# Kernel tuning notes

Hardware: AMD Instinct MI355X
Metric: run time of the kernel (lower is better)

## Reference

```python
import jax, jax.numpy as jnp
import numpy as np

NUM_NODES = 64   # EEG channels / input size
D = 512          # rnn1 hidden size
N_LAYERS = 3
B, T = 32, 1024


def _lstm_dir(x, W_ih, W_hh, b_ih, b_hh, reverse=False):
    """Single-direction LSTM layer (torch gate order i,f,g,o).
    x: [B,T,I], W_ih: [4H,I], W_hh: [4H,H], biases: [4H]. Returns [B,T,H]."""
    H = W_hh.shape[1]
    # Precompute input projection for all timesteps (big GEMM, compute-bound).
    xp = jnp.einsum('bti,gi->btg', x, W_ih) + (b_ih + b_hh)  # [B,T,4H]

    def step(carry, xt):
        h, c = carry
        gates = xt + h @ W_hh.T                 # [B,4H]
        i, f, g, o = jnp.split(gates, 4, axis=-1)
        i = jax.nn.sigmoid(i)
        f = jax.nn.sigmoid(f)
        g = jnp.tanh(g)
        o = jax.nn.sigmoid(o)
        c = f * c + i * g
        h = o * jnp.tanh(c)
        return (h, c), h

    init = (jnp.zeros((x.shape[0], H), x.dtype), jnp.zeros((x.shape[0], H), x.dtype))
    _, hs = jax.lax.scan(step, init, jnp.swapaxes(xp, 0, 1), reverse=reverse)
    return jnp.swapaxes(hs, 0, 1)  # [B,T,H]


def _bilstm(x, W_ih, W_hh, b_ih, b_hh):
    """Bidirectional layer; params stacked on leading dir axis [2,...]."""
    fwd = _lstm_dir(x, W_ih[0], W_hh[0], b_ih[0], b_hh[0], reverse=False)
    bwd = _lstm_dir(x, W_ih[1], W_hh[1], b_ih[1], b_hh[1], reverse=True)
    return jnp.concatenate([fwd, bwd], axis=-1)  # [B,T,2H]


def setup_inputs() -> dict:
    key = jax.random.key(0)
    ks = jax.random.split(key, 16)
    k1 = 1.0 / np.sqrt(D)          # torch LSTM init bound for rnn1
    k2 = 1.0 / np.sqrt(NUM_NODES)  # for rnn2
    u = lambda k, shape, b: jax.random.uniform(k, shape, jnp.float32, -b, b)
    inp = {
        'x': jax.random.normal(ks[0], (B, T, NUM_NODES), jnp.float32),
        # rnn1 layer 0: input NUM_NODES, 2 directions
        'W_ih_l0': u(ks[1], (2, 4 * D, NUM_NODES), k1),
        'W_hh_l0': u(ks[2], (2, 4 * D, D), k1),
        'b_ih_l0': u(ks[3], (2, 4 * D), k1),
        'b_hh_l0': u(ks[4], (2, 4 * D), k1),
        # rnn1 layers 1-2: input 2*D, stacked [layer, dir, ...]
        'W_ih_l12': u(ks[5], (2, 2, 4 * D, 2 * D), k1),
        'W_hh_l12': u(ks[6], (2, 2, 4 * D, D), k1),
        'b_ih_l12': u(ks[7], (2, 2, 4 * D), k1),
        'b_hh_l12': u(ks[8], (2, 2, 4 * D), k1),
        # rnn2: single unidirectional layer, input 2*D, hidden NUM_NODES
        'W_ih2': u(ks[9], (4 * NUM_NODES, 2 * D), k2),
        'W_hh2': u(ks[10], (4 * NUM_NODES, NUM_NODES), k2),
        'b_ih2': u(ks[11], (4 * NUM_NODES,), k2),
        'b_hh2': u(ks[12], (4 * NUM_NODES,), k2),
    }
    return inp


def reference(x, W_ih_l0, W_hh_l0, b_ih_l0, b_hh_l0,
              W_ih_l12, W_hh_l12, b_ih_l12, b_hh_l12,
              W_ih2, W_hh2, b_ih2, b_hh2):
    out = _bilstm(x, W_ih_l0, W_hh_l0, b_ih_l0, b_hh_l0)        # [B,T,2D]
    for l in range(N_LAYERS - 1):
        out = _bilstm(out, W_ih_l12[l], W_hh_l12[l], b_ih_l12[l], b_hh_l12[l])
    out = _lstm_dir(out, W_ih2, W_hh2, b_ih2, b_hh2)            # [B,T,NUM_NODES]
    return out * 40.0
```

## Files before the change

kernel.cpp:

```cpp
#include <hip/hip_runtime.h>
#include <stdio.h>
#include <stdint.h>

#define BB 32
#define TT 1024
#define DH 512
#define ND 64
#define TC 128

typedef short bf16x8 __attribute__((ext_vector_type(8)));
typedef float f32x4  __attribute__((ext_vector_type(4)));

static __device__ __forceinline__ float bf2f(unsigned short u) {
    union { unsigned int i; float f; } v; v.i = ((unsigned int)u) << 16; return v.f;
}
static __device__ __forceinline__ unsigned short f2bf_rne(float f) {
    union { float f; unsigned int i; } v; v.f = f;
    unsigned int u = v.i;
    return (unsigned short)((u + 0x7fffu + ((u >> 16) & 1u)) >> 16);
}
static __device__ __forceinline__ float sigm(float x) { return 1.f / (1.f + __expf(-x)); }
static __device__ __forceinline__ float tanhs(float x) {
    float ax = fabsf(x);
    float e = __expf(-2.f * ax);
    float t = (1.f - e) / (1.f + e);
    return x < 0.f ? -t : t;
}

__global__ void k_f2bf(const float* __restrict__ src, unsigned short* __restrict__ dst, int n4) {
    int i = blockIdx.x * blockDim.x + threadIdx.x;
    if (i < n4) {
        float4 v = ((const float4*)src)[i];
        ushort4 o;
        o.x = f2bf_rne(v.x); o.y = f2bf_rne(v.y); o.z = f2bf_rne(v.z); o.w = f2bf_rne(v.w);
        ((ushort4*)dst)[i] = o;
    }
}

__global__ void k_bsum(const float* __restrict__ a, const float* __restrict__ b,
                       float* __restrict__ d, int n) {
    int i = blockIdx.x * blockDim.x + threadIdx.x;
    if (i < n) d[i] = a[i] + b[i];
}

__global__ __launch_bounds__(256) void k_gemm(
    const unsigned short* __restrict__ A,
    const unsigned short* __restrict__ W,
    const float* __restrict__ bias,
    unsigned short* __restrict__ out,
    int N, int K)
{
    __shared__ unsigned short lw[128 * 72];
    __shared__ unsigned short la[128 * 72];
    const int tid = threadIdx.x;
    const int n0 = blockIdx.x * 128;
    const int m0 = blockIdx.y * 128;
    const int lane = tid & 63, wv = tid >> 6;
    const int q = lane >> 4, lr = lane & 15;
    const int wn = wv & 1, wm = wv >> 1;

    f32x4 acc[4][4];
#pragma unroll
    for (int i = 0; i < 4; i++)
#pragma unroll
        for (int j = 0; j < 4; j++) acc[i][j] = (f32x4){0.f, 0.f, 0.f, 0.f};

    const int srow = tid >> 1, shalf = tid & 1;
    for (int k0 = 0; k0 < K; k0 += 64) {
        const uint4* gw = (const uint4*)(W + (size_t)(n0 + srow) * K + k0 + shalf * 32);
        const uint4* ga = (const uint4*)(A + (size_t)(m0 + srow) * K + k0 + shalf * 32);
        uint4 wld[4], ald[4];
#pragma unroll
        for (int j = 0; j < 4; j++) { wld[j] = gw[j]; ald[j] = ga[j]; }
        __syncthreads();
#pragma unroll
        for (int j = 0; j < 4; j++) {
            ((uint4*)lw)[srow * 9 + shalf * 4 + j] = wld[j];
            ((uint4*)la)[srow * 9 + shalf * 4 + j] = ald[j];
        }
        __syncthreads();
#pragma unroll
        for (int ks = 0; ks < 2; ks++) {
            bf16x8 fw[4], fa[4];
#pragma unroll
            for (int i = 0; i < 4; i++)
                fw[i] = *(const bf16x8*)&lw[(64 * wn + 16 * i + lr) * 72 + ks * 32 + q * 8];
#pragma unroll
            for (int j = 0; j < 4; j++)
                fa[j] = *(const bf16x8*)&la[(64 * wm + 16 * j + lr) * 72 + ks * 32 + q * 8];
#pragma unroll
            for (int i = 0; i < 4; i++)
#pragma unroll
                for (int j = 0; j < 4; j++)
                    acc[i][j] = __builtin_amdgcn_mfma_f32_16x16x32_bf16(fw[i], fa[j], acc[i][j], 0, 0, 0);
        }
    }
#pragma unroll
    for (int i = 0; i < 4; i++) {
        const int nb = n0 + 64 * wn + 16 * i + q * 4;
        const float4 bb = *(const float4*)(bias + nb);
#pragma unroll
        for (int j = 0; j < 4; j++) {
            const int m = m0 + 64 * wm + 16 * j + lr;
            const int rowp = ((m & 1023) << 5) | (m >> 10);
            ushort4 o;
            o.x = f2bf_rne(acc[i][j][0] + bb.x);
            o.y = f2bf_rne(acc[i][j][1] + bb.y);
            o.z = f2bf_rne(acc[i][j][2] + bb.z);
            o.w = f2bf_rne(acc[i][j][3] + bb.w);
            *(ushort4*)(out + (size_t)rowp * N + nb) = o;
        }
    }
}

__global__ __launch_bounds__(512) void k_layer(
    const unsigned short* A,
    const unsigned short* wih,
    const float* bias,
    const unsigned short* whh,
    unsigned short* __restrict__ outb,
    unsigned short* xpc,
    unsigned short* hbuf,
    unsigned int* ctl, int K)
{
    extern __shared__ unsigned short smem[];
    const int tid = threadIdx.x;
    const int bid = blockIdx.x;
    unsigned int* chunkready = ctl;
    unsigned int* rnnprog = ctl + 128;
    unsigned int* stepflag = ctl + 256;

    if (bid < 64) {
        unsigned short* lw = smem;
        unsigned short* lh = smem + 128 * 520;
        float* lg = (float*)(smem + 128 * 520 + 16 * 520);
        const int dir = bid & 1;
        const int bg = (bid >> 1) & 1;
        const int cs = bid >> 2;
        const int c0 = cs * 32, b0 = bg * 16;
        const int lane = tid & 63, wv = tid >> 6;
        const int q = lane >> 4, lr = lane & 15;

        for (int i = tid; i < 128 * 64; i += 512) {
            int row = i >> 6, ch = i & 63;
            int ty = row >> 5, cc = row & 31;
            ((uint4*)lw)[row * 65 + ch] =
                *(const uint4*)(whh + ((size_t)(dir * 2048 + ty * 512 + c0 + cc) * 512 + ch * 8));
        }
        const int xb = tid >> 5;
        const int xc = tid & 31;
        float cstate = 0.f;
        unsigned int* myflag = stepflag + ((dir * 2 + bg) * 16 + cs) * 16;
        const unsigned int* grpflag = stepflag + (dir * 2 + bg) * 256;
        __syncthreads();

        for (int s = 0; s < TT; ++s) {
            if ((s & (TC - 1)) == 0) {
                const int c = s >> 7;
                if (tid == 0) {
                    while (__hip_atomic_load(&chunkready[c * 16], __ATOMIC_RELAXED,
                                             __HIP_MEMORY_SCOPE_AGENT) < 128u)
                        __builtin_amdgcn_s_sleep(8);
                }
                __syncthreads();
                __builtin_amdgcn_fence(__ATOMIC_ACQUIRE, "agent");
            }
            const unsigned short* xpb = xpc + (size_t)((s >> 7) & 1) * (TC * 32ull * 4096);
            const int t = dir ? (TT - 1 - s) : s;
            const unsigned short* xpp = xpb + ((size_t)((s & (TC - 1)) * 32 + b0 + xb) * 4096)
                                       + dir * 2048 + c0 + xc;
            unsigned short x0 = xpp[0], x1 = xpp[512], x2 = xpp[1024], x3 = xpp[1536];

            if (s > 0) {
                if (wv == 0) {
                    const unsigned int tgt = (unsigned int)s;
                    const unsigned int* fl = grpflag + (lane & 15) * 16;
                    for (;;) {
                        unsigned int v = (lane < 16)
                            ? __hip_atomic_load(fl, __ATOMIC_RELAXED, __HIP_MEMORY_SCOPE_AGENT)
                            : tgt;
                        if (__all((int)(v >= tgt))) break;
                    }
                }
                __syncthreads();
                {
                    const int pp = (s & 1) ^ 1;
                    const unsigned short* hb = hbuf + ((size_t)(dir * 2 + pp) * 32 + b0) * 512;
                    const int ch = tid & 127, r0 = tid >> 7;
                    unsigned long long hv4[4];
#pragma unroll
                    for (int k2 = 0; k2 < 4; ++k2)
                        hv4[k2] = __hip_atomic_load(
                            (const unsigned long long*)(hb + (r0 + k2 * 4) * 512 + ch * 4),
                            __ATOMIC_RELAXED, __HIP_MEMORY_SCOPE_AGENT);
#pragma unroll
                    for (int k2 = 0; k2 < 4; ++k2)
                        *(unsigned long long*)&((unsigned int*)lh)[(r0 + k2 * 4) * 260 + ch * 2] = hv4[k2];
                }
                __syncthreads();
                f32x4 acc = (f32x4){0.f, 0.f, 0.f, 0.f};
                const unsigned short* lwr = lw + (16 * wv + lr) * 520;
                const unsigned short* lhr = lh + lr * 520;
#pragma unroll
                for (int ks = 0; ks < 16; ++ks) {
                    bf16x8 a = *(const bf16x8*)(lwr + ks * 32 + q * 8);
                    bf16x8 b = *(const bf16x8*)(lhr + ks * 32 + q * 8);
                    acc = __builtin_amdgcn_mfma_f32_16x16x32_bf16(a, b, acc, 0, 0, 0);
                }
#pragma unroll
                for (int r = 0; r < 4; ++r)
                    lg[(16 * wv + q * 4 + r) * 17 + lr] = acc[r];
                __syncthreads();
            }

            unsigned short h16;
            {
                float gi = bf2f(x0) + (s > 0 ? lg[(0 * 32 + xc) * 17 + xb] : 0.f);
                float gf = bf2f(x1) + (s > 0 ? lg[(1 * 32 + xc) * 17 + xb] : 0.f);
                float gg = bf2f(x2) + (s > 0 ? lg[(2 * 32 + xc) * 17 + xb] : 0.f);
                float go = bf2f(x3) + (s > 0 ? lg[(3 * 32 + xc) * 17 + xb] : 0.f);
                float ig = sigm(gi), fg = sigm(gf), cg = tanhs(gg), og = sigm(go);
                cstate = fg * cstate + ig * cg;
                float h = og * tanhs(cstate);
                h16 = f2bf_rne(h);
                unsigned int hv = h16;
                unsigned int other = __shfl_xor((int)hv, 1);
                if ((tid & 1) == 0) {
                    size_t idx = ((size_t)(dir * 2 + (s & 1)) * 32 + b0 + xb) * 512 + c0 + xc;
                    unsigned int packed = hv | (other << 16);
                    __hip_atomic_store((unsigned int*)hbuf + (idx >> 1), packed,
                                       __ATOMIC_RELAXED, __HIP_MEMORY_SCOPE_AGENT);
                }
            }
            __syncthreads();
            if (tid == 0)
                __hip_atomic_store(myflag, (unsigned int)(s + 1),
                                   __ATOMIC_RELAXED, __HIP_MEMORY_SCOPE_AGENT);
            if ((s & (TC - 1)) == (TC - 1) && tid == 0)
                __hip_atomic_fetch_add(rnnprog, 1u, __ATOMIC_RELAXED, __HIP_MEMORY_SCOPE_AGENT);
            outb[((size_t)(b0 + xb) * TT + t) * 1024 + dir * 512 + c0 + xc] = h16;
        }
    } else {
        const int w = bid - 64;
        const int engine = tid >> 8;
        const int etid = tid & 255;
        unsigned short* lw = smem + engine * 18432;
        unsigned short* la = lw + 9216;
        const int lane = etid & 63, wv = etid >> 6;
        const int q = lane >> 4, lr = lane & 15;
        const int wn = wv & 1, wm = wv >> 1;
        const int srow = etid >> 1, shalf = etid & 1;

        for (int c = 0; c < 8; ++c) {
            if (c >= 2) {
                if (tid == 0) {
                    unsigned int tgt = 64u * (unsigned int)(c - 1);
                    while (__hip_atomic_load(rnnprog, __ATOMIC_RELAXED,
                                             __HIP_MEMORY_SCOPE_AGENT) < tgt)
                        __builtin_amdgcn_s_sleep(8);
                }
                __syncthreads();
            }
            unsigned short* xpb = xpc + (size_t)(c & 1) * (TC * 32ull * 4096);
            for (int jt = 0; jt < 4; ++jt) {
                const int tau = (w * 2 + engine) + 256 * jt;
                const int dir = tau >> 9, rem = tau & 511;
                const int b = rem >> 4, nx = rem & 15;
                const int t0 = dir ? (TT - c * TC - TC) : (c * TC);
                const int n0 = dir * 2048 + nx * 128;
                const int m0 = b * TT + t0;
                f32x4 acc[4][4];
#pragma unroll
                for (int i = 0; i < 4; i++)
#pragma unroll
                    for (int j = 0; j < 4; j++) acc[i][j] = (f32x4){0.f, 0.f, 0.f, 0.f};

                for (int k0 = 0; k0 < K; k0 += 64) {
                    const uint4* gw = (const uint4*)(wih + (size_t)(n0 + srow) * K + k0 + shalf * 32);
                    const uint4* ga = (const uint4*)(A + (size_t)(m0 + srow) * K + k0 + shalf * 32);
                    uint4 wld[4], ald[4];
#pragma unroll
                    for (int j = 0; j < 4; j++) { wld[j] = gw[j]; ald[j] = ga[j]; }
                    __syncthreads();
#pragma unroll
                    for (int j = 0; j < 4; j++) {
                        ((uint4*)lw)[srow * 9 + shalf * 4 + j] = wld[j];
                        ((uint4*)la)[srow * 9 + shalf * 4 + j] = ald[j];
                    }
                    __syncthreads();
#pragma unroll
                    for (int ks = 0; ks < 2; ks++) {
                        bf16x8 fw[4], fa[4];
#pragma unroll
                        for (int i = 0; i < 4; i++)
                            fw[i] = *(const bf16x8*)&lw[(64 * wn + 16 * i + lr) * 72 + ks * 32 + q * 8];
#pragma unroll
                        for (int j = 0; j < 4; j++)
                            fa[j] = *(const bf16x8*)&la[(64 * wm + 16 * j + lr) * 72 + ks * 32 + q * 8];
#pragma unroll
                        for (int i = 0; i < 4; i++)
#pragma unroll
                            for (int j = 0; j < 4; j++)
                                acc[i][j] = __builtin_amdgcn_mfma_f32_16x16x32_bf16(fw[i], fa[j], acc[i][j], 0, 0, 0);
                    }
                }
#pragma unroll
                for (int i = 0; i < 4; i++) {
                    const int nb = n0 + 64 * wn + 16 * i + q * 4;
                    const float4 bb = *(const float4*)(bias + nb);
#pragma unroll
                    for (int j = 0; j < 4; j++) {
                        const int dm = 64 * wm + 16 * j + lr;
                        const int islot = dir ? (TC - 1 - dm) : dm;
                        ushort4 o;
                        o.x = f2bf_rne(acc[i][j][0] + bb.x);
                        o.y = f2bf_rne(acc[i][j][1] + bb.y);
                        o.z = f2bf_rne(acc[i][j][2] + bb.z);
                        o.w = f2bf_rne(acc[i][j][3] + bb.w);
                        *(ushort4*)(xpb + ((size_t)islot * 32 + b) * 4096 + nb) = o;
                    }
                }
            }
            __builtin_amdgcn_fence(__ATOMIC_RELEASE, "agent");
            __syncthreads();
            if (tid == 0)
                __hip_atomic_fetch_add(&chunkready[c * 16], 1u,
                                       __ATOMIC_RELEASE, __HIP_MEMORY_SCOPE_AGENT);
        }
    }
}

__global__ __launch_bounds__(512) void k_rnn2(
    const unsigned short* __restrict__ xp2,
    const unsigned short* __restrict__ whh2,
    float* __restrict__ out)
{
    __shared__ unsigned short lw[256 * 72];
    __shared__ unsigned short lh[2][16 * 68];
    const int tid = threadIdx.x;
    const int b0 = blockIdx.x * 16;
    const int lane = tid & 63, wv = tid >> 6;
    const int q = lane >> 4, l = lane & 15;

    for (int i = tid; i < 256 * 8; i += 512) {
        int row = i >> 3, ch = i & 7;
        ((uint4*)lw)[row * 9 + ch] = *(const uint4*)(whh2 + (size_t)row * 64 + ch * 8);
    }
    __syncthreads();

    if (wv < 4) {
        const int cbase = wv * 16 + q * 4;
        float cst[4] = {0.f, 0.f, 0.f, 0.f};
        for (int s = 0; s < TT; ++s) {
            const unsigned short* xr = xp2 + (size_t)(s * 32 + b0 + l) * 256 + cbase;
            ushort4 xv0 = *(const ushort4*)(xr);
            ushort4 xv1 = *(const ushort4*)(xr + 64);
            ushort4 xv2 = *(const ushort4*)(xr + 128);
            ushort4 xv3 = *(const ushort4*)(xr + 192);
            f32x4 acc[4];
            if (s > 0) {
                const unsigned short* lhr = lh[(s & 1) ^ 1] + l * 68;
                bf16x8 hb0 = *(const bf16x8*)(lhr + q * 8);
                bf16x8 hb1 = *(const bf16x8*)(lhr + 32 + q * 8);
#pragma unroll
                for (int ty = 0; ty < 4; ++ty) {
                    const unsigned short* lwr = lw + (size_t)(ty * 64 + wv * 16 + l) * 72;
                    bf16x8 a0 = *(const bf16x8*)(lwr + q * 8);
                    bf16x8 a1 = *(const bf16x8*)(lwr + 32 + q * 8);
                    f32x4 tacc = (f32x4){0.f, 0.f, 0.f, 0.f};
                    tacc = __builtin_amdgcn_mfma_f32_16x16x32_bf16(a0, hb0, tacc, 0, 0, 0);
                    tacc = __builtin_amdgcn_mfma_f32_16x16x32_bf16(a1, hb1, tacc, 0, 0, 0);
                    acc[ty] = tacc;
                }
            } else {
#pragma unroll
                for (int ty = 0; ty < 4; ++ty) acc[ty] = (f32x4){0.f, 0.f, 0.f, 0.f};
            }
            ushort4 ho; float4 oo;
            const unsigned short* xs0 = (const unsigned short*)&xv0;
            const unsigned short* xs1 = (const unsigned short*)&xv1;
            const unsigned short* xs2 = (const unsigned short*)&xv2;
            const unsigned short* xs3 = (const unsigned short*)&xv3;
#pragma unroll
            for (int r = 0; r < 4; ++r) {
                float gi = bf2f(xs0[r]) + acc[0][r];
                float gf = bf2f(xs1[r]) + acc[1][r];
                float gg = bf2f(xs2[r]) + acc[2][r];
                float go = bf2f(xs3[r]) + acc[3][r];
                float ig = sigm(gi), fg = sigm(gf), cg = tanhs(gg), og = sigm(go);
                cst[r] = fg * cst[r] + ig * cg;
                float h = og * tanhs(cst[r]);
                ((float*)&oo)[r] = 40.f * h;
                ((unsigned short*)&ho)[r] = f2bf_rne(h);
            }
            *(ushort4*)(lh[s & 1] + l * 68 + cbase) = ho;
            *(float4*)(out + ((size_t)(b0 + l) * TT + s) * 64 + cbase) = oo;
            __syncthreads();
        }
    } else {
        for (int s = 0; s < TT; ++s) __syncthreads();
    }
}

extern "C" void kernel_launch(void* const* d_in, const int* in_sizes, int n_in,
                              void* d_out, int out_size, void* d_ws, size_t ws_size,
                              hipStream_t stream) {
    (void)in_sizes; (void)n_in; (void)out_size;
    const float* x     = (const float*)d_in[0];
    const float* Wih0  = (const float*)d_in[1];
    const float* Whh0  = (const float*)d_in[2];
    const float* bih0  = (const float*)d_in[3];
    const float* bhh0  = (const float*)d_in[4];
    const float* Wih12 = (const float*)d_in[5];
    const float* Whh12 = (const float*)d_in[6];
    const float* bih12 = (const float*)d_in[7];
    const float* bhh12 = (const float*)d_in[8];
    const float* Wih2  = (const float*)d_in[9];
    const float* Whh2  = (const float*)d_in[10];
    const float* bih2  = (const float*)d_in[11];
    const float* bhh2  = (const float*)d_in[12];
    float* out = (float*)d_out;

    char* ws = (char*)d_ws;
    size_t off = 0;
    auto alloc = [&](size_t sz) { char* p = ws + off; off += (sz + 255) & ~(size_t)255; return p; };
    unsigned short* actA  = (unsigned short*)alloc(33554432ull * 2);
    unsigned short* actB  = (unsigned short*)alloc(33554432ull * 2);
    unsigned short* xpc   = (unsigned short*)alloc(2ull * TC * 32 * 4096 * 2);
    unsigned short* xbf   = (unsigned short*)alloc(2097152ull * 2);
    unsigned short* wihc  = (unsigned short*)alloc(4194304ull * 2);
    unsigned short* whhc  = (unsigned short*)alloc(2097152ull * 2);
    unsigned short* wih2b = (unsigned short*)alloc(262144ull * 2);
    unsigned short* whh2b = (unsigned short*)alloc(16384ull * 2);
    float* bs  = (float*)alloc(4096 * 4);
    float* bs2 = (float*)alloc(256 * 4);
    unsigned short* hbuf = (unsigned short*)alloc(2ull * 2 * 32 * 512 * 2);
    unsigned int* ctrl = (unsigned int*)alloc(16384);

    if (ws_size < off) {
        fprintf(stderr, "[kernel_launch] ws_size=%zu < needed=%zu — aborting cleanly\n", ws_size, off);
        return;
    }

    auto cvt = [&](const float* s, unsigned short* d, int n) {
        int n4 = n / 4;
        k_f2bf<<<(n4 + 255) / 256, 256, 0, stream>>>(s, d, n4);
    };
    cvt(x, xbf, 2097152);
    cvt(Wih2, wih2b, 262144);
    cvt(Whh2, whh2b, 16384);
    k_bsum<<<1, 256, 0, stream>>>(bih2, bhh2, bs2, 256);

    hipError_t rc = hipFuncSetAttribute(reinterpret_cast<const void*>(k_layer),
                                        hipFuncAttributeMaxDynamicSharedMemorySize, 160 * 1024);
    if (rc != hipSuccess) fprintf(stderr, "[kernel_launch] hipFuncSetAttribute rc=%d\n", (int)rc);
    const size_t layer_lds = (size_t)(128 * 520 + 16 * 520) * 2 + (size_t)128 * 17 * 4;

    for (int l = 0; l < 3; ++l) {
        const unsigned short* Abuf;
        unsigned short* Obuf;
        int K;
        if (l == 0) {
            cvt(Wih0, wihc, 262144);
            cvt(Whh0, whhc, 2097152);
            k_bsum<<<16, 256, 0, stream>>>(bih0, bhh0, bs, 4096);
            Abuf = xbf; Obuf = actA; K = 64;
        } else {
            cvt(Wih12 + (size_t)(l - 1) * 4194304, wihc, 4194304);
            cvt(Whh12 + (size_t)(l - 1) * 2097152, whhc, 2097152);
            k_bsum<<<16, 256, 0, stream>>>(bih12 + (l - 1) * 4096, bhh12 + (l - 1) * 4096, bs, 4096);
            Abuf = (l == 1) ? actA : actB;
            Obuf = (l == 1) ? actB : actA;
            K = 1024;
        }
        hipMemsetAsync(ctrl, 0, 16384, stream);
        k_layer<<<192, 512, layer_lds, stream>>>(Abuf, wihc, bs, whhc, Obuf, xpc, hbuf, ctrl, K);
    }

    k_gemm<<<dim3(2, 256), 256, 0, stream>>>(actA, wih2b, bs2, xpc, 256, 1024);
    k_rnn2<<<2, 512, 0, stream>>>(xpc, whh2b, out);
}
```

Before: 11.46 ms.

## Replace per-step flag barrier with sentinel-tagged triple-buffered hidden state

Drops the per-step flag counters and block barrier that signalled hidden-state readiness. Consumers now poll the hidden-state buffer itself until no word equals a 0xFFFFFFFF sentinel. A third buffer slot lets each block reset the next slot to the sentinel while others still read the previous one. This cuts a global flag round trip and a __syncthreads per timestep from the serial recurrence, but relies on a bf16 pair never encoding the sentinel and on the ordering of relaxed atomics between the data and sentinel stores.

New measurement: 14.01 ms. +22.3%, slower.

```diff
diff --git a/kernel.cpp b/kernel.cpp
--- a/kernel.cpp
+++ b/kernel.cpp
@@ -7,6 +7,7 @@
 #define DH 512
 #define ND 64
 #define TC 128
+#define SENT32 0xFFFFFFFFu
 
 typedef short bf16x8 __attribute__((ext_vector_type(8)));
 typedef float f32x4  __attribute__((ext_vector_type(4)));
@@ -128,7 +129,6 @@
     const int bid = blockIdx.x;
     unsigned int* chunkready = ctl;
     unsigned int* rnnprog = ctl + 128;
-    unsigned int* stepflag = ctl + 256;
 
     if (bid < 64) {
         unsigned short* lw = smem;
@@ -150,11 +150,12 @@
         const int xb = tid >> 5;
         const int xc = tid & 31;
         float cstate = 0.f;
-        unsigned int* myflag = stepflag + ((dir * 2 + bg) * 16 + cs) * 16;
-        const unsigned int* grpflag = stepflag + (dir * 2 + bg) * 256;
         __syncthreads();
 
+        int pw = 0;
         for (int s = 0; s < TT; ++s) {
+            const int pr = (pw == 0) ? 2 : pw - 1;
+            const int pn = (pw == 2) ? 0 : pw + 1;
             if ((s & (TC - 1)) == 0) {
                 const int c = s >> 7;
                 if (tid == 0) {
@@ -172,31 +173,33 @@
             unsigned short x0 = xpp[0], x1 = xpp[512], x2 = xpp[1024], x3 = xpp[1536];
 
             if (s > 0) {
-                if (wv == 0) {
-                    const unsigned int tgt = (unsigned int)s;
-                    const unsigned int* fl = grpflag + (lane & 15) * 16;
-                    for (;;) {
-                        unsigned int v = (lane < 16)
-                            ? __hip_atomic_load(fl, __ATOMIC_RELAXED, __HIP_MEMORY_SCOPE_AGENT)
-                            : tgt;
-                        if (__all((int)(v >= tgt))) break;
-                    }
-                }
-                __syncthreads();
-                {
-                    const int pp = (s & 1) ^ 1;
-                    const unsigned short* hb = hbuf + ((size_t)(dir * 2 + pp) * 32 + b0) * 512;
-                    const int ch = tid & 127, r0 = tid >> 7;
-                    unsigned long long hv4[4];
+                const unsigned short* hb = hbuf + ((size_t)(dir * 3 + pr) * 32 + b0) * 512;
+                const int ch = tid & 127, r0 = tid >> 7;
+                unsigned long long hv4[4];
+                unsigned int done = 0;
+                do {
 #pragma unroll
                     for (int k2 = 0; k2 < 4; ++k2)
-                        hv4[k2] = __hip_atomic_load(
-                            (const unsigned long long*)(hb + (r0 + k2 * 4) * 512 + ch * 4),
-                            __ATOMIC_RELAXED, __HIP_MEMORY_SCOPE_AGENT);
+                        if (!((done >> k2) & 1u))
+                            hv4[k2] = __hip_atomic_load(
+                                (const unsigned long long*)(hb + (r0 + k2 * 4) * 512 + ch * 4),
+                                __ATOMIC_RELAXED, __HIP_MEMORY_SCOPE_AGENT);
 #pragma unroll
                     for (int k2 = 0; k2 < 4; ++k2)
-                        *(unsigned long long*)&((unsigned int*)lh)[(r0 + k2 * 4) * 260 + ch * 2] = hv4[k2];
-                }
+                        if (!((done >> k2) & 1u)) {
+                            unsigned int lo = (unsigned int)hv4[k2];
+                            unsigned int hi = (unsigned int)(hv4[k2] >> 32);
+                            if (lo != SENT32 && hi != SENT32) done |= 1u << k2;
+                        }
+                } while (done != 15u);
+                if ((tid & 1) == 0) {
+                    size_t idx = ((size_t)(dir * 3 + pn) * 32 + b0 + xb) * 512 + c0 + xc;
+                    __hip_atomic_store((unsigned int*)hbuf + (idx >> 1), SENT32,
+                                       __ATOMIC_RELAXED, __HIP_MEMORY_SCOPE_AGENT);
+                }
+#pragma unroll
+                for (int k2 = 0; k2 < 4; ++k2)
+                    *(unsigned long long*)&((unsigned int*)lh)[(r0 + k2 * 4) * 260 + ch * 2] = hv4[k2];
                 __syncthreads();
                 f32x4 acc = (f32x4){0.f, 0.f, 0.f, 0.f};
                 const unsigned short* lwr = lw + (16 * wv + lr) * 520;
@@ -211,6 +214,12 @@
                 for (int r = 0; r < 4; ++r)
                     lg[(16 * wv + q * 4 + r) * 17 + lr] = acc[r];
                 __syncthreads();
+            } else {
+                if ((tid & 1) == 0) {
+                    size_t idx = ((size_t)(dir * 3 + pn) * 32 + b0 + xb) * 512 + c0 + xc;
+                    __hip_atomic_store((unsigned int*)hbuf + (idx >> 1), SENT32,
+                                       __ATOMIC_RELAXED, __HIP_MEMORY_SCOPE_AGENT);
+                }
             }
 
             unsigned short h16;
@@ -226,19 +235,20 @@
                 unsigned int hv = h16;
                 unsigned int other = __shfl_xor((int)hv, 1);
                 if ((tid & 1) == 0) {
-                    size_t idx = ((size_t)(dir * 2 + (s & 1)) * 32 + b0 + xb) * 512 + c0 + xc;
+                    size_t idx = ((size_t)(dir * 3 + pw) * 32 + b0 + xb) * 512 + c0 + xc;
                     unsigned int packed = hv | (other << 16);
                     __hip_atomic_store((unsigned int*)hbuf + (idx >> 1), packed,
                                        __ATOMIC_RELAXED, __HIP_MEMORY_SCOPE_AGENT);
                 }
             }
-            __syncthreads();
-            if (tid == 0)
-                __hip_atomic_store(myflag, (unsigned int)(s + 1),
-                                   __ATOMIC_RELAXED, __HIP_MEMORY_SCOPE_AGENT);
-            if ((s & (TC - 1)) == (TC - 1) && tid == 0)
-                __hip_atomic_fetch_add(rnnprog, 1u, __ATOMIC_RELAXED, __HIP_MEMORY_SCOPE_AGENT);
             outb[((size_t)(b0 + xb) * TT + t) * 1024 + dir * 512 + c0 + xc] = h16;
+
+            if ((s & (TC - 1)) == (TC - 1)) {
+                __syncthreads();
+                if (tid == 0)
+                    __hip_atomic_fetch_add(rnnprog, 1u, __ATOMIC_RELAXED, __HIP_MEMORY_SCOPE_AGENT);
+            }
+            pw = pn;
         }
     } else {
         const int w = bid - 64;
@@ -434,7 +444,7 @@
     unsigned short* whh2b = (unsigned short*)alloc(16384ull * 2);
     float* bs  = (float*)alloc(4096 * 4);
     float* bs2 = (float*)alloc(256 * 4);
-    unsigned short* hbuf = (unsigned short*)alloc(2ull * 2 * 32 * 512 * 2);
+    unsigned short* hbuf = (unsigned short*)alloc(2ull * 3 * 32 * 512 * 2);
     unsigned int* ctrl = (unsigned int*)alloc(16384);
 
     if (ws_size < off) {
@@ -474,6 +484,7 @@
             K = 1024;
         }
         hipMemsetAsync(ctrl, 0, 16384, stream);
+        hipMemsetAsync(hbuf, 0xFF, 2ull * 3 * 32 * 512 * 2, stream);
         k_layer<<<192, 512, layer_lds, stream>>>(Abuf, wihc, bs, whhc, Obuf, xpc, hbuf, ctrl, K);
     }
 
```
